# Kernel optimization log

Measured on AMD Instinct MI355X. Metric: run time of the kernel, lower is better.

The kernel has to match this reference:

```python
import jax, jax.numpy as jnp
import numpy as np

HEADS = 16
D_MODEL = 1024
HEAD_DIM = D_MODEL // HEADS
NEG = -1e15


def setup_inputs() -> dict:
    key = jax.random.key(0)
    ks = jax.random.split(key, 13)
    B, L = 2, 2048
    scale = 1.0 / np.sqrt(D_MODEL)
    inp = {
        'q': jax.random.normal(ks[0], (B, L, D_MODEL), jnp.float32),
        'k': jax.random.normal(ks[1], (B, L, D_MODEL), jnp.float32),
        'v': jax.random.normal(ks[2], (B, L, D_MODEL), jnp.float32),
        'mask': jax.random.randint(ks[3], (B, 1, 1, L), 0, 2, jnp.int32),
        'Wq': jax.random.normal(ks[4], (D_MODEL, D_MODEL), jnp.float32) * scale,
        'bq': jax.random.normal(ks[5], (D_MODEL,), jnp.float32) * scale,
        'Wk': jax.random.normal(ks[6], (D_MODEL, D_MODEL), jnp.float32) * scale,
        'bk': jax.random.normal(ks[7], (D_MODEL,), jnp.float32) * scale,
        'Wv': jax.random.normal(ks[8], (D_MODEL, D_MODEL), jnp.float32) * scale,
        'bv': jax.random.normal(ks[9], (D_MODEL,), jnp.float32) * scale,
        'Wo': jax.random.normal(ks[10], (D_MODEL, D_MODEL), jnp.float32) * scale,
        'bo': jax.random.normal(ks[11], (D_MODEL,), jnp.float32) * scale,
    }
    return inp


def _split_heads(x):
    B, L, _ = x.shape
    return x.reshape(B, L, HEADS, HEAD_DIM).transpose(0, 2, 1, 3)  # [B,H,L,Dh]


def reference(q, k, v, mask, Wq, bq, Wk, bk, Wv, bv, Wo, bo):
    B, L, _ = q.shape
    # torch Linear: y = x @ W.T + b
    qh = _split_heads(q @ Wq.T + bq)
    kh = _split_heads(k @ Wk.T + bk)
    vh = _split_heads(v @ Wv.T + bv)
    scores = jnp.einsum('bhqd,bhkd->bhqk', qh, kh) / jnp.sqrt(jnp.float32(HEAD_DIM))
    scores = scores + mask.astype(scores.dtype) * NEG
    weights = jax.nn.softmax(scores, axis=-1)
    attn = jnp.einsum('bhqk,bhkd->bhqd', weights, vh)  # [B,H,L,Dh]
    attn = attn.transpose(0, 2, 1, 3).reshape(B, L, D_MODEL)
    return attn @ Wo.T + bo
```

## Files before the change

### kernel.cpp

```cpp
#include <hip/hip_runtime.h>
#include <stdint.h>

typedef __bf16 bf16;
typedef __attribute__((ext_vector_type(8))) __bf16 bf16x8;
typedef __attribute__((ext_vector_type(4))) __bf16 bf16x4;
typedef __attribute__((ext_vector_type(4))) float f32x4;

#define SEQ   2048
#define DM    1024
#define NH    16
#define HD    64
#define MROWS 4096

__device__ __forceinline__ void glds16(const bf16* g, bf16* l) {
  __builtin_amdgcn_global_load_lds(
      (__attribute__((address_space(1))) unsigned int*)(g),
      (__attribute__((address_space(3))) unsigned int*)(l),
      16, 0, 0);
}

static __device__ __forceinline__ bf16x8 cvt_f32x8(const float* __restrict__ p) {
  const f32x4 a = *(const f32x4*)p;
  const f32x4 b = *(const f32x4*)(p + 4);
  bf16x8 r;
  r[0] = (bf16)a[0]; r[1] = (bf16)a[1]; r[2] = (bf16)a[2]; r[3] = (bf16)a[3];
  r[4] = (bf16)b[0]; r[5] = (bf16)b[1]; r[6] = (bf16)b[2]; r[7] = (bf16)b[3];
  return r;
}

__global__ void conv_all(
    const float* __restrict__ q, const float* __restrict__ k, const float* __restrict__ v,
    const float* __restrict__ wq, const float* __restrict__ wk,
    const float* __restrict__ wv, const float* __restrict__ wo,
    bf16* __restrict__ dq, bf16* __restrict__ dk, bf16* __restrict__ dv,
    bf16* __restrict__ dwq, bf16* __restrict__ dwk, bf16* __restrict__ dwv,
    bf16* __restrict__ dwo)
{
  const size_t c = (size_t)blockIdx.x * 256 + threadIdx.x;
  const float* s; bf16* d; size_t off;
  if (c < 524288)        { s = q;  d = dq;  off = c; }
  else if (c < 1048576)  { s = k;  d = dk;  off = c - 524288; }
  else if (c < 1572864)  { s = v;  d = dv;  off = c - 1048576; }
  else if (c < 1703936)  { s = wq; d = dwq; off = c - 1572864; }
  else if (c < 1835008)  { s = wk; d = dwk; off = c - 1703936; }
  else if (c < 1966080)  { s = wv; d = dwv; off = c - 1835008; }
  else                   { s = wo; d = dwo; off = c - 1966080; }
  *(bf16x8*)(d + off * 8) = cvt_f32x8(s + off * 8);
}

__global__ __launch_bounds__(256, 4) void proj_qkv(
    const bf16* __restrict__ qb, const bf16* __restrict__ kb, const bf16* __restrict__ vb,
    const bf16* __restrict__ Wqb, const bf16* __restrict__ Wkb, const bf16* __restrict__ Wvb,
    const float* __restrict__ bq, const float* __restrict__ bk, const float* __restrict__ bv,
    bf16* __restrict__ Qh, bf16* __restrict__ Kh, bf16* __restrict__ Vt)
{
  __shared__ __align__(16) bf16 sA[128 * 64];
  __shared__ __align__(16) bf16 sB[128 * 64];

  const int z = blockIdx.z;
  const int o = (int)blockIdx.x + 8 * (int)blockIdx.y;
  const int rt = (o & 7) * 4 + ((o >> 3) & 3);
  const int ot = o >> 5;

  const bf16 *A, *B;
  const float* Bv;
  int m0, n0;
  if (z == 0)      { A = qb;  B = Wqb; Bv = bq; m0 = rt * 128; n0 = ot * 128; }
  else if (z == 1) { A = kb;  B = Wkb; Bv = bk; m0 = rt * 128; n0 = ot * 128; }
  else             { A = Wvb; B = vb;  Bv = bv; m0 = ot * 128; n0 = rt * 128; }

  const int tid  = threadIdx.x;
  const int lane = tid & 63;
  const int wv   = tid >> 6;
  const int quad = lane >> 4;
  const int colx = lane & 15;
  const int rm = (wv >> 1) * 64;
  const int rn = (wv & 1) * 64;

  f32x4 acc[4][4];
#pragma unroll
  for (int mi = 0; mi < 4; ++mi)
#pragma unroll
    for (int ni = 0; ni < 4; ++ni) {
      f32x4 zz = {0.f, 0.f, 0.f, 0.f};
      acc[mi][ni] = zz;
    }

  for (int kt = 0; kt < 16; ++kt) {
    const int k0 = kt * 64;
    __syncthreads();
#pragma unroll
    for (int i = 0; i < 4; ++i) {
      const int f = i * 256 + tid;
      const int row = f >> 3;
      const int cc = (f & 7) ^ (row & 7);
      glds16(A + (size_t)(m0 + row) * DM + k0 + cc * 8, sA + f * 8);
      glds16(B + (size_t)(n0 + row) * DM + k0 + cc * 8, sB + f * 8);
    }
    __syncthreads();

    bf16x8 af[4][2], bfr[4][2];
#pragma unroll
    for (int t4 = 0; t4 < 4; ++t4) {
#pragma unroll
      for (int ks = 0; ks < 2; ++ks) {
        const int ra = rm + t4 * 16 + colx;
        af[t4][ks] = *(const bf16x8*)(sA + ra * 64 + (((ks * 4 + quad) ^ (ra & 7)) * 8));
        const int rb = rn + t4 * 16 + colx;
        bfr[t4][ks] = *(const bf16x8*)(sB + rb * 64 + (((ks * 4 + quad) ^ (rb & 7)) * 8));
      }
    }
#pragma unroll
    for (int mi = 0; mi < 4; ++mi)
#pragma unroll
      for (int ni = 0; ni < 4; ++ni) {
        acc[mi][ni] = __builtin_amdgcn_mfma_f32_16x16x32_bf16(af[mi][0], bfr[ni][0], acc[mi][ni], 0, 0, 0);
        acc[mi][ni] = __builtin_amdgcn_mfma_f32_16x16x32_bf16(af[mi][1], bfr[ni][1], acc[mi][ni], 0, 0, 0);
      }
  }

  if (z == 2) {
#pragma unroll
    for (int mi = 0; mi < 4; ++mi) {
#pragma unroll
      for (int r = 0; r < 4; ++r) {
        const int m = m0 + rm + mi * 16 + quad * 4 + r;
        const float bias = Bv[m];
        const int hh = m >> 6, d = m & 63;
#pragma unroll
        for (int ni = 0; ni < 4; ++ni) {
          const int n = n0 + rn + ni * 16 + colx;
          const int b = n >> 11, l = n & 2047;
          const int lb = l >> 7, li = l & 127;
          const int perm = (li & 96) | ((li & 12) << 1) | ((li & 16) >> 2) | (li & 3);
          Vt[(((size_t)(b * NH + hh) * HD + d) * SEQ) + lb * 128 + perm] =
              (bf16)(acc[mi][ni][r] + bias);
        }
      }
    }
  } else {
    bf16* Out = (z == 0) ? Qh : Kh;
    const float scale = (z == 0) ? 0.18033688f : 1.0f;
#pragma unroll
    for (int ni = 0; ni < 4; ++ni) {
      const int n = n0 + rn + ni * 16 + colx;
      const float bias = Bv[n];
#pragma unroll
      for (int mi = 0; mi < 4; ++mi) {
#pragma unroll
        for (int r = 0; r < 4; ++r) {
          const int m = m0 + rm + mi * 16 + quad * 4 + r;
          const float v = (acc[mi][ni][r] + bias) * scale;
          const int b = m >> 11, l = m & 2047, hh = n >> 6, d = n & 63;
          Out[((size_t)(b * NH + hh) * SEQ + l) * HD + d] = (bf16)v;
        }
      }
    }
  }
}

__global__ __launch_bounds__(256, 4) void proj_out(
    const bf16* __restrict__ At, const bf16* __restrict__ Wob,
    const float* __restrict__ bo, float* __restrict__ Out)
{
  __shared__ __align__(16) bf16 sA[128 * 64];
  __shared__ __align__(16) bf16 sB[128 * 64];

  const int o = (int)blockIdx.x + 8 * (int)blockIdx.y;
  const int m0 = ((o & 7) * 4 + ((o >> 3) & 3)) * 128;
  const int n0 = (o >> 5) * 128;

  const int tid  = threadIdx.x;
  const int lane = tid & 63;
  const int wv   = tid >> 6;
  const int quad = lane >> 4;
  const int colx = lane & 15;
  const int rm = (wv >> 1) * 64;
  const int rn = (wv & 1) * 64;

  f32x4 acc[4][4];
#pragma unroll
  for (int mi = 0; mi < 4; ++mi)
#pragma unroll
    for (int ni = 0; ni < 4; ++ni) {
      f32x4 zz = {0.f, 0.f, 0.f, 0.f};
      acc[mi][ni] = zz;
    }

  for (int kt = 0; kt < 16; ++kt) {
    const int k0 = kt * 64;
    __syncthreads();
#pragma unroll
    for (int i = 0; i < 4; ++i) {
      const int f = i * 256 + tid;
      const int row = f >> 3;
      const int cc = (f & 7) ^ (row & 7);
      glds16(At  + (size_t)(m0 + row) * DM + k0 + cc * 8, sA + f * 8);
      glds16(Wob + (size_t)(n0 + row) * DM + k0 + cc * 8, sB + f * 8);
    }
    __syncthreads();

    bf16x8 af[4][2], bfr[4][2];
#pragma unroll
    for (int t4 = 0; t4 < 4; ++t4) {
#pragma unroll
      for (int ks = 0; ks < 2; ++ks) {
        const int ra = rm + t4 * 16 + colx;
        af[t4][ks] = *(const bf16x8*)(sA + ra * 64 + (((ks * 4 + quad) ^ (ra & 7)) * 8));
        const int rb = rn + t4 * 16 + colx;
        bfr[t4][ks] = *(const bf16x8*)(sB + rb * 64 + (((ks * 4 + quad) ^ (rb & 7)) * 8));
      }
    }
#pragma unroll
    for (int mi = 0; mi < 4; ++mi)
#pragma unroll
      for (int ni = 0; ni < 4; ++ni) {
        acc[mi][ni] = __builtin_amdgcn_mfma_f32_16x16x32_bf16(af[mi][0], bfr[ni][0], acc[mi][ni], 0, 0, 0);
        acc[mi][ni] = __builtin_amdgcn_mfma_f32_16x16x32_bf16(af[mi][1], bfr[ni][1], acc[mi][ni], 0, 0, 0);
      }
  }

#pragma unroll
  for (int ni = 0; ni < 4; ++ni) {
    const int n = n0 + rn + ni * 16 + colx;
    const float bias = bo[n];
#pragma unroll
    for (int mi = 0; mi < 4; ++mi) {
#pragma unroll
      for (int r = 0; r < 4; ++r) {
        const int m = m0 + rm + mi * 16 + quad * 4 + r;
        Out[(size_t)m * DM + n] = acc[mi][ni][r] + bias;
      }
    }
  }
}

__global__ __launch_bounds__(256, 3) void attn_kernel(
    const bf16* __restrict__ Qh, const bf16* __restrict__ Kh, const bf16* __restrict__ Vt,
    const int* __restrict__ mask, bf16* __restrict__ At)
{
  __shared__ __align__(16) char smem[32768];
  bf16* sK = (bf16*)smem;
  bf16* sV = (bf16*)(smem + 16384);

  const int tid  = threadIdx.x;
  const int lane = tid & 63;
  const int wv   = tid >> 6;
  const int quad = lane >> 4;
  const int colx = lane & 15;
  const int bh = blockIdx.x;
  const int b  = bh >> 4;
  const int h  = bh & 15;
  const int q0 = blockIdx.y * 64;
  const size_t base  = (size_t)bh * SEQ * HD;
  const size_t baseV = (size_t)bh * HD * SEQ;

  bf16x8 qf[4][2];
#pragma unroll
  for (int qg = 0; qg < 4; ++qg) {
    const int qrow = q0 + qg * 16 + colx;
    qf[qg][0] = *(const bf16x8*)(Qh + base + (size_t)qrow * HD + quad * 8);
    qf[qg][1] = *(const bf16x8*)(Qh + base + (size_t)qrow * HD + 32 + quad * 8);
  }

  f32x4 o[4][4];
  float osum[4];
#pragma unroll
  for (int qg = 0; qg < 4; ++qg) {
    osum[qg] = 0.f;
#pragma unroll
    for (int dt = 0; dt < 4; ++dt) {
      f32x4 zz = {0.f, 0.f, 0.f, 0.f};
      o[qg][dt] = zz;
    }
  }

  union VV { bf16x8 v8; bf16x4 v4[2]; };

  for (int t = 0; t < 16; ++t) {
    const int key0 = t * 128;
    __syncthreads();
#pragma unroll
    for (int i = 0; i < 4; ++i) {
      const int f = i * 256 + tid;
      const int kr = f >> 3;
      const int ck = (f & 7) ^ (kr & 7);
      glds16(Kh + base + (size_t)(key0 + kr) * HD + ck * 8, sK + f * 8);
      const int dr = f >> 4;
      const int cv = (f & 15) ^ (dr & 15);
      glds16(Vt + baseV + (size_t)dr * SEQ + key0 + cv * 8, sV + f * 8);
    }
    const int kb = key0 + wv * 32;
    const int4 mA = *(const int4*)(mask + b * SEQ + kb + quad * 4);
    const int4 mB = *(const int4*)(mask + b * SEQ + kb + 16 + quad * 4);
    float mr0[4], mr1[4];
    mr0[0] = (mA.x ? -1e30f : 0.0f) - 23.0830917f;
    mr0[1] = (mA.y ? -1e30f : 0.0f) - 23.0830917f;
    mr0[2] = (mA.z ? -1e30f : 0.0f) - 23.0830917f;
    mr0[3] = (mA.w ? -1e30f : 0.0f) - 23.0830917f;
    mr1[0] = (mB.x ? -1e30f : 0.0f) - 23.0830917f;
    mr1[1] = (mB.y ? -1e30f : 0.0f) - 23.0830917f;
    mr1[2] = (mB.z ? -1e30f : 0.0f) - 23.0830917f;
    mr1[3] = (mB.w ? -1e30f : 0.0f) - 23.0830917f;
    __syncthreads();

    VV pa[4];
    __builtin_amdgcn_s_setprio(1);
#pragma unroll
    for (int g = 0; g < 2; ++g) {
      const int krow = wv * 32 + g * 16 + colx;
      const bf16x8 kfa = *(const bf16x8*)(sK + krow * 64 + ((quad ^ (krow & 7)) * 8));
      const bf16x8 kfb = *(const bf16x8*)(sK + krow * 64 + (((4 + quad) ^ (krow & 7)) * 8));
#pragma unroll
      for (int qg = 0; qg < 4; ++qg) {
        f32x4 s = {0.f, 0.f, 0.f, 0.f};
        s = __builtin_amdgcn_mfma_f32_16x16x32_bf16(kfa, qf[qg][0], s, 0, 0, 0);
        s = __builtin_amdgcn_mfma_f32_16x16x32_bf16(kfb, qf[qg][1], s, 0, 0, 0);
#pragma unroll
        for (int r = 0; r < 4; ++r) {
          const float e = __builtin_amdgcn_exp2f(s[r] + (g ? mr1[r] : mr0[r]));
          pa[qg].v8[g * 4 + r] = (bf16)e;
          osum[qg] += e;
        }
      }
    }

    bf16x8 vf[4];
#pragma unroll
    for (int dt = 0; dt < 4; ++dt) {
      const int row = dt * 16 + colx;
      vf[dt] = *(const bf16x8*)(sV + row * 128 + (((wv * 4 + quad) ^ colx) * 8));
    }

#pragma unroll
    for (int dt = 0; dt < 4; ++dt)
#pragma unroll
      for (int qg = 0; qg < 4; ++qg)
        o[qg][dt] = __builtin_amdgcn_mfma_f32_16x16x32_bf16(pa[qg].v8, vf[dt], o[qg][dt], 0, 0, 0);
    __builtin_amdgcn_s_setprio(0);
  }

  __syncthreads();
  float* sRed = (float*)smem;
  float* sDen = (float*)(smem + 64 * 68 * 4);

#pragma unroll
  for (int qg = 0; qg < 4; ++qg) {
    osum[qg] += __shfl_xor(osum[qg], 16);
    osum[qg] += __shfl_xor(osum[qg], 32);
  }
  const float myden = (quad == 0) ? osum[0] : (quad == 1) ? osum[1]
                    : (quad == 2) ? osum[2] : osum[3];

#pragma unroll
  for (int p = 0; p < 4; ++p) {
    if (wv == p) {
#pragma unroll
      for (int qg = 0; qg < 4; ++qg)
#pragma unroll
        for (int dt = 0; dt < 4; ++dt) {
          float* a = &sRed[(dt * 16 + colx) * 68 + qg * 16 + quad * 4];
          if (p == 0) {
            *(f32x4*)a = o[qg][dt];
          } else {
            f32x4 c = *(const f32x4*)a;
            c += o[qg][dt];
            *(f32x4*)a = c;
          }
        }
      if (p == 0) sDen[quad * 16 + colx] = myden;
      else        sDen[quad * 16 + colx] += myden;
    }
    __syncthreads();
  }

  const float inv = 1.0f / sDen[wv * 16 + colx];
  bf16x8 out0, out1;
#pragma unroll
  for (int j = 0; j < 8; ++j) {
    out0[j] = (bf16)(sRed[(quad * 16 + j) * 68 + wv * 16 + colx] * inv);
    out1[j] = (bf16)(sRed[(quad * 16 + 8 + j) * 68 + wv * 16 + colx] * inv);
  }
  const size_t orow = ((size_t)(b * SEQ + q0 + wv * 16 + colx)) * DM + h * HD + quad * 16;
  *(bf16x8*)(At + orow) = out0;
  *(bf16x8*)(At + orow + 8) = out1;
}

extern "C" void kernel_launch(void* const* d_in, const int* in_sizes, int n_in,
                              void* d_out, int out_size, void* d_ws, size_t ws_size,
                              hipStream_t stream) {
  (void)in_sizes; (void)n_in; (void)out_size; (void)ws_size;
  const float* q    = (const float*)d_in[0];
  const float* k    = (const float*)d_in[1];
  const float* v    = (const float*)d_in[2];
  const int*   mask = (const int*)d_in[3];
  const float* Wq   = (const float*)d_in[4];
  const float* bq   = (const float*)d_in[5];
  const float* Wk   = (const float*)d_in[6];
  const float* bk   = (const float*)d_in[7];
  const float* Wv   = (const float*)d_in[8];
  const float* bv   = (const float*)d_in[9];
  const float* Wo   = (const float*)d_in[10];
  const float* bo   = (const float*)d_in[11];
  float* out = (float*)d_out;

  const size_t T = (size_t)MROWS * DM;
  const size_t WT = (size_t)DM * DM;
  bf16* ws  = (bf16*)d_ws;
  bf16* qb  = ws;
  bf16* kb  = qb + T;
  bf16* vb  = kb + T;
  bf16* Wqb = vb + T;
  bf16* Wkb = Wqb + WT;
  bf16* Wvb = Wkb + WT;
  bf16* Wob = Wvb + WT;
  bf16* Qh  = Wob + WT;
  bf16* Kh  = Qh + T;
  bf16* Vt  = Kh + T;
  bf16* At  = qb;

  dim3 blk(256);
  conv_all<<<8192, blk, 0, stream>>>(q, k, v, Wq, Wk, Wv, Wo,
                                     qb, kb, vb, Wqb, Wkb, Wvb, Wob);
  proj_qkv<<<dim3(8, 32, 3), blk, 0, stream>>>(qb, kb, vb, Wqb, Wkb, Wvb,
                                               bq, bk, bv, Qh, Kh, Vt);
  attn_kernel<<<dim3(32, 32), blk, 0, stream>>>(Qh, Kh, Vt, mask, At);
  proj_out<<<dim3(8, 32), blk, 0, stream>>>(At, Wob, bo, out);
}
```

Baseline: 245.0 us.

## Share K/V tiles across two query halves with 512-thread attention blocks

The attention block grows to 512 threads covering 128 query rows. Two groups of four waves each take 64 queries and share one K/V tile loaded into LDS, so each K/V tile is fetched half as often. Each thread now issues half as many global-to-LDS copies per tile. The grid is halved and the reduction buffers are doubled, which brings occupancy down to 2 blocks of 512 threads and raises LDS use.

```diff
diff --git a/kernel.cpp b/kernel.cpp
--- a/kernel.cpp
+++ b/kernel.cpp
@@ -3,7 +3,6 @@
 
 typedef __bf16 bf16;
 typedef __attribute__((ext_vector_type(8))) __bf16 bf16x8;
-typedef __attribute__((ext_vector_type(4))) __bf16 bf16x4;
 typedef __attribute__((ext_vector_type(4))) float f32x4;
 
 #define SEQ   2048
@@ -235,30 +234,32 @@
   }
 }
 
-__global__ __launch_bounds__(256, 3) void attn_kernel(
+__global__ __launch_bounds__(512, 2) void attn_kernel(
     const bf16* __restrict__ Qh, const bf16* __restrict__ Kh, const bf16* __restrict__ Vt,
     const int* __restrict__ mask, bf16* __restrict__ At)
 {
-  __shared__ __align__(16) char smem[32768];
+  __shared__ __align__(16) char smem[35840];
   bf16* sK = (bf16*)smem;
   bf16* sV = (bf16*)(smem + 16384);
 
   const int tid  = threadIdx.x;
   const int lane = tid & 63;
   const int wv   = tid >> 6;
+  const int ks   = wv & 3;
+  const int qh   = wv >> 2;
   const int quad = lane >> 4;
   const int colx = lane & 15;
   const int bh = blockIdx.x;
   const int b  = bh >> 4;
   const int h  = bh & 15;
-  const int q0 = blockIdx.y * 64;
+  const int q0 = blockIdx.y * 128;
   const size_t base  = (size_t)bh * SEQ * HD;
   const size_t baseV = (size_t)bh * HD * SEQ;
 
   bf16x8 qf[4][2];
 #pragma unroll
   for (int qg = 0; qg < 4; ++qg) {
-    const int qrow = q0 + qg * 16 + colx;
+    const int qrow = q0 + qh * 64 + qg * 16 + colx;
     qf[qg][0] = *(const bf16x8*)(Qh + base + (size_t)qrow * HD + quad * 8);
     qf[qg][1] = *(const bf16x8*)(Qh + base + (size_t)qrow * HD + 32 + quad * 8);
   }
@@ -275,14 +276,12 @@
     }
   }
 
-  union VV { bf16x8 v8; bf16x4 v4[2]; };
-
   for (int t = 0; t < 16; ++t) {
     const int key0 = t * 128;
     __syncthreads();
 #pragma unroll
-    for (int i = 0; i < 4; ++i) {
-      const int f = i * 256 + tid;
+    for (int i = 0; i < 2; ++i) {
+      const int f = i * 512 + tid;
       const int kr = f >> 3;
       const int ck = (f & 7) ^ (kr & 7);
       glds16(Kh + base + (size_t)(key0 + kr) * HD + ck * 8, sK + f * 8);
@@ -290,7 +289,7 @@
       const int cv = (f & 15) ^ (dr & 15);
       glds16(Vt + baseV + (size_t)dr * SEQ + key0 + cv * 8, sV + f * 8);
     }
-    const int kb = key0 + wv * 32;
+    const int kb = key0 + ks * 32;
     const int4 mA = *(const int4*)(mask + b * SEQ + kb + quad * 4);
     const int4 mB = *(const int4*)(mask + b * SEQ + kb + 16 + quad * 4);
     float mr0[4], mr1[4];
@@ -304,11 +303,11 @@
     mr1[3] = (mB.w ? -1e30f : 0.0f) - 23.0830917f;
     __syncthreads();
 
-    VV pa[4];
+    bf16x8 pa[4];
     __builtin_amdgcn_s_setprio(1);
 #pragma unroll
     for (int g = 0; g < 2; ++g) {
-      const int krow = wv * 32 + g * 16 + colx;
+      const int krow = ks * 32 + g * 16 + colx;
       const bf16x8 kfa = *(const bf16x8*)(sK + krow * 64 + ((quad ^ (krow & 7)) * 8));
       const bf16x8 kfb = *(const bf16x8*)(sK + krow * 64 + (((4 + quad) ^ (krow & 7)) * 8));
 #pragma unroll
@@ -319,7 +318,7 @@
 #pragma unroll
         for (int r = 0; r < 4; ++r) {
           const float e = __builtin_amdgcn_exp2f(s[r] + (g ? mr1[r] : mr0[r]));
-          pa[qg].v8[g * 4 + r] = (bf16)e;
+          pa[qg][g * 4 + r] = (bf16)e;
           osum[qg] += e;
         }
       }
@@ -329,20 +328,20 @@
 #pragma unroll
     for (int dt = 0; dt < 4; ++dt) {
       const int row = dt * 16 + colx;
-      vf[dt] = *(const bf16x8*)(sV + row * 128 + (((wv * 4 + quad) ^ colx) * 8));
+      vf[dt] = *(const bf16x8*)(sV + row * 128 + (((ks * 4 + quad) ^ colx) * 8));
     }
 
 #pragma unroll
     for (int dt = 0; dt < 4; ++dt)
 #pragma unroll
       for (int qg = 0; qg < 4; ++qg)
-        o[qg][dt] = __builtin_amdgcn_mfma_f32_16x16x32_bf16(pa[qg].v8, vf[dt], o[qg][dt], 0, 0, 0);
+        o[qg][dt] = __builtin_amdgcn_mfma_f32_16x16x32_bf16(pa[qg], vf[dt], o[qg][dt], 0, 0, 0);
     __builtin_amdgcn_s_setprio(0);
   }
 
   __syncthreads();
-  float* sRed = (float*)smem;
-  float* sDen = (float*)(smem + 64 * 68 * 4);
+  float* sRedB = (float*)smem;
+  float* sDenB = (float*)(smem + 2 * 64 * 68 * 4);
 
 #pragma unroll
   for (int qg = 0; qg < 4; ++qg) {
@@ -352,14 +351,17 @@
   const float myden = (quad == 0) ? osum[0] : (quad == 1) ? osum[1]
                     : (quad == 2) ? osum[2] : osum[3];
 
+  float* red = sRedB + qh * 64 * 68;
+  float* den = sDenB + qh * 64;
+
 #pragma unroll
   for (int p = 0; p < 4; ++p) {
-    if (wv == p) {
+    if (ks == p) {
 #pragma unroll
       for (int qg = 0; qg < 4; ++qg)
 #pragma unroll
         for (int dt = 0; dt < 4; ++dt) {
-          float* a = &sRed[(dt * 16 + colx) * 68 + qg * 16 + quad * 4];
+          float* a = &red[(dt * 16 + colx) * 68 + qg * 16 + quad * 4];
           if (p == 0) {
             *(f32x4*)a = o[qg][dt];
           } else {
@@ -368,18 +370,19 @@
             *(f32x4*)a = c;
           }
         }
-      if (p == 0) sDen[quad * 16 + colx] = myden;
-      else        sDen[quad * 16 + colx] += myden;
-    }
-    __syncthreads();
-  }
-
-  const float inv = 1.0f / sDen[wv * 16 + colx];
+      if (p == 0) den[quad * 16 + colx] = myden;
+      else        den[quad * 16 + colx] += myden;
+    }
+    __syncthreads();
+  }
+
+  const float* redR = sRedB + (wv >> 2) * 64 * 68;
+  const float invd = 1.0f / (sDenB + (wv >> 2) * 64)[(wv & 3) * 16 + colx];
   bf16x8 out0, out1;
 #pragma unroll
   for (int j = 0; j < 8; ++j) {
-    out0[j] = (bf16)(sRed[(quad * 16 + j) * 68 + wv * 16 + colx] * inv);
-    out1[j] = (bf16)(sRed[(quad * 16 + 8 + j) * 68 + wv * 16 + colx] * inv);
+    out0[j] = (bf16)(redR[(quad * 16 + j) * 68 + (wv & 3) * 16 + colx] * invd);
+    out1[j] = (bf16)(redR[(quad * 16 + 8 + j) * 68 + (wv & 3) * 16 + colx] * invd);
   }
   const size_t orow = ((size_t)(b * SEQ + q0 + wv * 16 + colx)) * DM + h * HD + quad * 16;
   *(bf16x8*)(At + orow) = out0;
@@ -424,6 +427,6 @@
                                      qb, kb, vb, Wqb, Wkb, Wvb, Wob);
   proj_qkv<<<dim3(8, 32, 3), blk, 0, stream>>>(qb, kb, vb, Wqb, Wkb, Wvb,
                                                bq, bk, bv, Qh, Kh, Vt);
-  attn_kernel<<<dim3(32, 32), blk, 0, stream>>>(Qh, Kh, Vt, mask, At);
+  attn_kernel<<<dim3(32, 16), dim3(512), 0, stream>>>(Qh, Kh, Vt, mask, At);
   proj_out<<<dim3(8, 32), blk, 0, stream>>>(At, Wob, bo, out);
 }
```

New measurement: 233.8 us. 1.05x faster.
